# Performance work log

Measured on AMD Instinct MI355X. Metric: run time of the kernel, lower is better.

Reference implementation:

```python
import jax, jax.numpy as jnp
import numpy as np

N_LEAVES = 16384
D = 1024
L = 32


def _build_full_binary_tree(n_leaves):
    # Leaves are node ids [0, n_leaves); internal nodes are assigned ids level by
    # level bottom-up, so children always have smaller ids than their parent and
    # left_idx/right_idx are grouped contiguously per level.
    level_nodes = np.arange(n_leaves)
    nid = n_leaves
    lefts, rights = [], []
    while level_nodes.size > 1:
        lefts.append(level_nodes[0::2])
        rights.append(level_nodes[1::2])
        w = level_nodes.size // 2
        level_nodes = np.arange(nid, nid + w)
        nid += w
    return np.concatenate(lefts).astype(np.int32), np.concatenate(rights).astype(np.int32)


def setup_inputs() -> dict:
    key = jax.random.key(0)
    k_h, k_t, k_w = jax.random.split(key, 3)
    n_nodes = 2 * N_LEAVES - 1
    hidden = jax.random.normal(k_h, (n_nodes, D), dtype=jnp.float32)
    # xavier_normal-ish scales
    trans = jax.random.normal(k_t, (L, L), dtype=jnp.float32) * (2.0 / (L + L)) ** 0.5
    W_pred = jax.random.normal(k_w, (L, 2 * D), dtype=jnp.float32) * (2.0 / (2 * D + L)) ** 0.5
    b_pred = jnp.zeros((L,), dtype=jnp.float32)
    left_idx, right_idx = _build_full_binary_tree(N_LEAVES)
    return {
        "hidden": hidden,
        "trans": trans,
        "W_pred": W_pred,
        "b_pred": b_pred,
        "left_idx": jnp.asarray(left_idx),
        "right_idx": jnp.asarray(right_idx),
    }


def reference(hidden, trans, W_pred, b_pred, left_idx, right_idx):
    # hidden: [N, D] node bottom-up hidden states; N = 2*n_leaves - 1
    n_nodes, d = hidden.shape
    n_leaves = (n_nodes + 1) // 2
    num_labels = trans.shape[0]

    # collect_avg_hidden: mean over all node hidden states
    avg_h = jnp.mean(hidden, axis=0)  # [D]
    # avg_h_pred: emission = Linear(concat(h, avg_h))  -> [N, L]
    feats = jnp.concatenate(
        [hidden, jnp.broadcast_to(avg_h, hidden.shape)], axis=1
    )  # [N, 2D]
    emission = feats @ W_pred.T + b_pred  # [N, L]

    # Inside DP, bottom-up, batched by tree level. For an internal node p:
    #   inside[p, y] = logsumexp_{l,r}( emission[p,y] + trans[y,l] + inside_left[l]
    #                                   + trans[y,r] + inside_right[r] )
    # which factorizes exactly into two independent logsumexps.
    scores = jnp.zeros((n_nodes, num_labels), dtype=hidden.dtype)
    scores = scores.at[:n_leaves].set(emission[:n_leaves])

    pos = 0
    node_base = n_leaves
    width = n_leaves // 2
    while width >= 1:  # fixed log2(n_leaves) structural levels
        li = left_idx[pos:pos + width]
        ri = right_idx[pos:pos + width]
        ls = scores[li]  # [width, L]
        rs = scores[ri]  # [width, L]
        # trans[y, c] + child_score[c], logsumexp over child label c
        left_m = jax.nn.logsumexp(trans[None, :, :] + ls[:, None, :], axis=2)
        right_m = jax.nn.logsumexp(trans[None, :, :] + rs[:, None, :], axis=2)
        new = emission[node_base:node_base + width] + left_m + right_m
        scores = scores.at[node_base:node_base + width].set(new)
        pos += width
        node_base += width
        width //= 2

    return scores[n_nodes - 1]  # root inside score, [L]
```

## Files before the change

kernel.cpp:

```cpp
#include <hip/hip_runtime.h>

#define NN 32767
#define NL 16384
#define DD 1024
#define LL 32

typedef __attribute__((ext_vector_type(8))) short bf16x8;
typedef __attribute__((ext_vector_type(4))) float f32x4;

__device__ __forceinline__ short f2bf(float f) {
  union { float f; unsigned u; } x; x.f = f;
  unsigned r = x.u + 0x7FFFu + ((x.u >> 16) & 1u);
  return (short)(r >> 16);
}

__device__ __forceinline__ bf16x8 cvt8(float4 a, float4 b) {
  bf16x8 r;
  r[0] = f2bf(a.x); r[1] = f2bf(a.y); r[2] = f2bf(a.z); r[3] = f2bf(a.w);
  r[4] = f2bf(b.x); r[5] = f2bf(b.y); r[6] = f2bf(b.z); r[7] = f2bf(b.w);
  return r;
}

__device__ __forceinline__ void gld_lds16(const float* g, float* l) {
  __builtin_amdgcn_global_load_lds(
      (const __attribute__((address_space(1))) void*)g,
      (__attribute__((address_space(3))) void*)l, 16, 0, 0);
}

__global__ __launch_bounds__(256) void pack_kernel(const float* __restrict__ Wp,
                                                   short* __restrict__ Wpk) {
  int idx = blockIdx.x * 256 + threadIdx.x;
  #pragma unroll
  for (int t = 0; t < 4; ++t, idx += 16384) {
    const int j = idx & 7, m = (idx >> 3) & 3, lane = (idx >> 5) & 63, s = idx >> 11;
    const int wrow = (lane & 15) + 16 * (m & 1);
    const int wcol = (m >> 1) * 1024 + s * 32 + (lane >> 4) * 8 + j;
    Wpk[idx] = f2bf(Wp[(size_t)wrow * (2 * DD) + wcol]);
  }
}

__global__ __launch_bounds__(256) void gemm_kernel(
    const float* __restrict__ hidden, const short* __restrict__ Wpk,
    float* __restrict__ E0, float* __restrict__ gpart) {
  __shared__ float lds[4 * 3 * 1024];
  const int tid = threadIdx.x;
  const int wid = tid >> 6, lane = tid & 63;
  const int tile = blockIdx.x * 4 + wid;
  const int mrow = lane & 15, g = lane >> 4;
  const int swz = (mrow & 7) << 4;
  float* ldsw = lds + wid * 3072;

  const float* ab0; const float* ab1; const float* ab2; const float* ab3;
  {
    const int lr = lane >> 4, lc16 = (lane & 15) * 16;
    #define MKAB(I, P) { const int row = (I)*4 + lr;                         \
      const int csrc = lc16 ^ ((row & 7) << 4);                              \
      int grow = tile * 16 + row; if (grow > NN - 1) grow = NN - 1;          \
      P = hidden + (size_t)grow * DD + (csrc >> 2); }
    MKAB(0, ab0) MKAB(1, ab1) MKAB(2, ab2) MKAB(3, ab3)
    #undef MKAB
  }
  const bf16x8* wbase = (const bf16x8*)Wpk + (size_t)lane * 4;

  const int cidx00 = ((g * 32) ^ swz) >> 2;
  const int cidx01 = ((g * 32 + 16) ^ swz) >> 2;
  const int cidx10 = ((128 + g * 32) ^ swz) >> 2;
  const int cidx11 = ((128 + g * 32 + 16) ^ swz) >> 2;

  f32x4 acc0 = {0,0,0,0}, acc1 = {0,0,0,0}, acc2 = {0,0,0,0}, acc3 = {0,0,0,0};

#define STAGE_A(KC) {                                   \
    float* ld_ = ldsw + ((KC) % 3) * 1024;              \
    gld_lds16(ab0 + (KC) * 64, ld_);                    \
    gld_lds16(ab1 + (KC) * 64, ld_ + 256);              \
    gld_lds16(ab2 + (KC) * 64, ld_ + 512);              \
    gld_lds16(ab3 + (KC) * 64, ld_ + 768); }

#define LOAD_W(KC, W0,W1,W2,W3, X0,X1,X2,X3) {          \
    const bf16x8* p_ = wbase + (size_t)(2 * (KC)) * 256; \
    W0 = p_[0];   W1 = p_[1];   W2 = p_[2];   W3 = p_[3]; \
    X0 = p_[256]; X1 = p_[257]; X2 = p_[258]; X3 = p_[259]; }

#define CHUNK(KC, VM, W0,W1,W2,W3, X0,X1,X2,X3)                              \
  { if ((KC) + 2 < 16) STAGE_A((KC) + 2)                                     \
    asm volatile("s_waitcnt vmcnt(" VM ")" ::: "memory");                    \
    { const float* bc = ldsw + ((KC) % 3) * 1024 + mrow * 64;                \
      float4 fa0 = *(const float4*)(bc + cidx00);                            \
      float4 fb0 = *(const float4*)(bc + cidx01);                            \
      bf16x8 af0 = cvt8(fa0, fb0);                                           \
      acc0 = __builtin_amdgcn_mfma_f32_16x16x32_bf16(af0, W0, acc0, 0,0,0);  \
      acc1 = __builtin_amdgcn_mfma_f32_16x16x32_bf16(af0, W1, acc1, 0,0,0);  \
      acc2 = __builtin_amdgcn_mfma_f32_16x16x32_bf16(af0, W2, acc2, 0,0,0);  \
      acc3 = __builtin_amdgcn_mfma_f32_16x16x32_bf16(af0, W3, acc3, 0,0,0);  \
      float4 fa1 = *(const float4*)(bc + cidx10);                            \
      float4 fb1 = *(const float4*)(bc + cidx11);                            \
      bf16x8 af1 = cvt8(fa1, fb1);                                           \
      acc0 = __builtin_amdgcn_mfma_f32_16x16x32_bf16(af1, X0, acc0, 0,0,0);  \
      acc1 = __builtin_amdgcn_mfma_f32_16x16x32_bf16(af1, X1, acc1, 0,0,0);  \
      acc2 = __builtin_amdgcn_mfma_f32_16x16x32_bf16(af1, X2, acc2, 0,0,0);  \
      acc3 = __builtin_amdgcn_mfma_f32_16x16x32_bf16(af1, X3, acc3, 0,0,0);  \
    }                                                                        \
    if ((KC) + 2 < 16) LOAD_W((KC) + 2, W0,W1,W2,W3, X0,X1,X2,X3) }

  bf16x8 u0,u1,u2,u3,u4,u5,u6,u7, v0,v1,v2,v3,v4,v5,v6,v7;
  STAGE_A(0) STAGE_A(1)
  LOAD_W(0, u0,u1,u2,u3, u4,u5,u6,u7)
  LOAD_W(1, v0,v1,v2,v3, v4,v5,v6,v7)
  CHUNK( 0, "24", u0,u1,u2,u3, u4,u5,u6,u7)
  CHUNK( 1, "32", v0,v1,v2,v3, v4,v5,v6,v7)
  CHUNK( 2, "24", u0,u1,u2,u3, u4,u5,u6,u7)
  CHUNK( 3, "24", v0,v1,v2,v3, v4,v5,v6,v7)
  CHUNK( 4, "24", u0,u1,u2,u3, u4,u5,u6,u7)
  CHUNK( 5, "24", v0,v1,v2,v3, v4,v5,v6,v7)
  CHUNK( 6, "24", u0,u1,u2,u3, u4,u5,u6,u7)
  CHUNK( 7, "24", v0,v1,v2,v3, v4,v5,v6,v7)
  CHUNK( 8, "24", u0,u1,u2,u3, u4,u5,u6,u7)
  CHUNK( 9, "24", v0,v1,v2,v3, v4,v5,v6,v7)
  CHUNK(10, "24", u0,u1,u2,u3, u4,u5,u6,u7)
  CHUNK(11, "24", v0,v1,v2,v3, v4,v5,v6,v7)
  CHUNK(12, "24", u0,u1,u2,u3, u4,u5,u6,u7)
  CHUNK(13, "24", v0,v1,v2,v3, v4,v5,v6,v7)
  CHUNK(14, "20", u0,u1,u2,u3, u4,u5,u6,u7)
  CHUNK(15, "8",  v0,v1,v2,v3, v4,v5,v6,v7)
#undef CHUNK
#undef LOAD_W
#undef STAGE_A

  #pragma unroll
  for (int r = 0; r < 4; ++r) {
    const int srow = tile * 16 + g * 4 + r;
    if (srow < NN) {
      E0[(size_t)srow * LL + mrow]      = acc0[r];
      E0[(size_t)srow * LL + mrow + 16] = acc1[r];
    }
  }
  if (tile == 2047 && g == 3) { acc2[3] = 0.f; acc3[3] = 0.f; }
  float s2 = acc2[0] + acc2[1] + acc2[2] + acc2[3];
  float s3 = acc3[0] + acc3[1] + acc3[2] + acc3[3];
  s2 += __shfl_xor(s2, 16, 64); s2 += __shfl_xor(s2, 32, 64);
  s3 += __shfl_xor(s3, 16, 64); s3 += __shfl_xor(s3, 32, 64);
  if (lane < 32) gpart[(size_t)tile * LL + lane] = (lane < 16) ? s2 : s3;
}

__global__ __launch_bounds__(256) void cvec_kernel(
    const float* __restrict__ bp, const float* __restrict__ gpart,
    float* __restrict__ cvec) {
  const int col = blockIdx.x;
  const int tid = threadIdx.x, wid = tid >> 6, lane = tid & 63;
  float s = 0.f;
  for (int w = tid; w < 2048; w += 256) s += gpart[(size_t)w * LL + col];
  #pragma unroll
  for (int m = 1; m <= 32; m <<= 1) s += __shfl_xor(s, m, 64);
  __shared__ float red[4];
  if (lane == 0) red[wid] = s;
  __syncthreads();
  if (tid == 0)
    cvec[col] = bp[col] + (red[0] + red[1] + red[2] + red[3]) * (1.0f / (float)NN);
}

__device__ __forceinline__ float lse32(const float4* tt, const float4* sv) {
  float m = -3.0e38f;
  float4 v[8];
  #pragma unroll
  for (int i = 0; i < 8; ++i) {
    float4 t = tt[i], s = sv[i], w;
    w.x = t.x + s.x; w.y = t.y + s.y; w.z = t.z + s.z; w.w = t.w + s.w;
    v[i] = w;
    m = fmaxf(m, fmaxf(fmaxf(w.x, w.y), fmaxf(w.z, w.w)));
  }
  float ss = 0.f;
  #pragma unroll
  for (int i = 0; i < 8; ++i) {
    ss += __expf(v[i].x - m) + __expf(v[i].y - m) +
          __expf(v[i].z - m) + __expf(v[i].w - m);
  }
  return m + __logf(ss);
}

__global__ __launch_bounds__(1024) void tree_kernel(
    const float* __restrict__ E0, const float* __restrict__ cvec,
    const float* __restrict__ trans, const float* __restrict__ src,
    float* __restrict__ dst, int base1, int leafmode) {
  __shared__ float l1[16][LL], l2[8][LL], l3[4][LL];
  const int wid = threadIdx.x >> 6, lane = threadIdx.x & 63;
  const int j = lane & 31, half = lane >> 5;
  const int b = blockIdx.x, G = gridDim.x;
  float4 tt[8];
  #pragma unroll
  for (int i = 0; i < 8; ++i) tt[i] = *(const float4*)(trans + j * LL + i * 4);
  const float cj = cvec[j];
  float4 sv[8];

  {
    const int n = b * 16 + wid;
    const float* sp = src + (size_t)(2 * n + half) * LL;
    if (leafmode) {
      #pragma unroll
      for (int i = 0; i < 8; ++i) {
        float4 vv = *(const float4*)(sp + i * 4);
        float4 c4 = *(const float4*)(cvec + i * 4);
        vv.x += c4.x; vv.y += c4.y; vv.z += c4.z; vv.w += c4.w;
        sv[i] = vv;
      }
    } else {
      #pragma unroll
      for (int i = 0; i < 8; ++i) sv[i] = *(const float4*)(sp + i * 4);
    }
    float lsum = lse32(tt, sv);
    float other = __shfl_xor(lsum, 32, 64);
    float o = E0[(size_t)(base1 + n) * LL + j] + cj + lsum + other;
    if (lane < 32) l1[wid][j] = o;
  }
  __syncthreads();
  const int base2 = base1 + G * 16;
  if (wid < 8) {
    const float* sp = l1[2 * wid + half];
    #pragma unroll
    for (int i = 0; i < 8; ++i) sv[i] = *(const float4*)(sp + i * 4);
    float lsum = lse32(tt, sv);
    float other = __shfl_xor(lsum, 32, 64);
    float o = E0[(size_t)(base2 + b * 8 + wid) * LL + j] + cj + lsum + other;
    if (lane < 32) l2[wid][j] = o;
  }
  __syncthreads();
  const int base3 = base2 + G * 8;
  if (wid < 4) {
    const float* sp = l2[2 * wid + half];
    #pragma unroll
    for (int i = 0; i < 8; ++i) sv[i] = *(const float4*)(sp + i * 4);
    float lsum = lse32(tt, sv);
    float other = __shfl_xor(lsum, 32, 64);
    float o = E0[(size_t)(base3 + b * 4 + wid) * LL + j] + cj + lsum + other;
    if (lane < 32) l3[wid][j] = o;
  }
  __syncthreads();
  const int base4 = base3 + G * 4;
  if (wid < 2) {
    const float* sp = l3[2 * wid + half];
    #pragma unroll
    for (int i = 0; i < 8; ++i) sv[i] = *(const float4*)(sp + i * 4);
    float lsum = lse32(tt, sv);
    float other = __shfl_xor(lsum, 32, 64);
    float o = E0[(size_t)(base4 + b * 2 + wid) * LL + j] + cj + lsum + other;
    if (lane < 32) l1[wid][j] = o;
  }
  __syncthreads();
  const int base5 = base4 + G * 2;
  if (wid == 0) {
    const float* sp = l1[half];
    #pragma unroll
    for (int i = 0; i < 8; ++i) sv[i] = *(const float4*)(sp + i * 4);
    float lsum = lse32(tt, sv);
    float other = __shfl_xor(lsum, 32, 64);
    float o = E0[(size_t)(base5 + b) * LL + j] + cj + lsum + other;
    if (lane < 32) dst[(size_t)b * LL + j] = o;
  }
}

__global__ __launch_bounds__(512) void tail_kernel(
    const float* __restrict__ E0, const float* __restrict__ cvec,
    const float* __restrict__ trans, const float* __restrict__ S10,
    float* __restrict__ out) {
  __shared__ float t1[8][LL], t2[4][LL], t3[2][LL];
  const int wid = threadIdx.x >> 6, lane = threadIdx.x & 63;
  const int j = lane & 31, half = lane >> 5;
  float4 tt[8];
  #pragma unroll
  for (int i = 0; i < 8; ++i) tt[i] = *(const float4*)(trans + j * LL + i * 4);
  const float cj = cvec[j];
  float4 sv[8];

  {
    const float* sp = S10 + (size_t)(2 * wid + half) * LL;
    #pragma unroll
    for (int i = 0; i < 8; ++i) sv[i] = *(const float4*)(sp + i * 4);
    float lsum = lse32(tt, sv);
    float other = __shfl_xor(lsum, 32, 64);
    float o = E0[(size_t)(32752 + wid) * LL + j] + cj + lsum + other;
    if (lane < 32) t1[wid][j] = o;
  }
  __syncthreads();
  if (wid < 4) {
    const float* sp = t1[2 * wid + half];
    #pragma unroll
    for (int i = 0; i < 8; ++i) sv[i] = *(const float4*)(sp + i * 4);
    float lsum = lse32(tt, sv);
    float other = __shfl_xor(lsum, 32, 64);
    float o = E0[(size_t)(32760 + wid) * LL + j] + cj + lsum + other;
    if (lane < 32) t2[wid][j] = o;
  }
  __syncthreads();
  if (wid < 2) {
    const float* sp = t2[2 * wid + half];
    #pragma unroll
    for (int i = 0; i < 8; ++i) sv[i] = *(const float4*)(sp + i * 4);
    float lsum = lse32(tt, sv);
    float other = __shfl_xor(lsum, 32, 64);
    float o = E0[(size_t)(32764 + wid) * LL + j] + cj + lsum + other;
    if (lane < 32) t3[wid][j] = o;
  }
  __syncthreads();
  if (wid == 0) {
    const float* sp = t3[half];
    #pragma unroll
    for (int i = 0; i < 8; ++i) sv[i] = *(const float4*)(sp + i * 4);
    float lsum = lse32(tt, sv);
    float other = __shfl_xor(lsum, 32, 64);
    float o = E0[(size_t)32766 * LL + j] + cj + lsum + other;
    if (lane < 32) out[j] = o;
  }
}

extern "C" void kernel_launch(void* const* d_in, const int* in_sizes, int n_in,
                              void* d_out, int out_size, void* d_ws, size_t ws_size,
                              hipStream_t stream) {
  const float* hidden = (const float*)d_in[0];
  const float* trans  = (const float*)d_in[1];
  const float* Wp     = (const float*)d_in[2];
  const float* bp     = (const float*)d_in[3];

  float* ws    = (float*)d_ws;
  float* E0    = ws;
  float* gpart = E0 + (size_t)NN * LL;
  float* cvecb = gpart + (size_t)2048 * LL;
  float* S5    = cvecb + 32;
  float* S10   = S5 + 512 * LL;
  short* Wpk   = (short*)(S10 + 16 * LL);

  pack_kernel<<<64, 256, 0, stream>>>(Wp, Wpk);
  gemm_kernel<<<512, 256, 0, stream>>>(hidden, Wpk, E0, gpart);
  cvec_kernel<<<32, 256, 0, stream>>>(bp, gpart, cvecb);
  tree_kernel<<<512, 1024, 0, stream>>>(E0, cvecb, trans, E0, S5, 16384, 1);
  tree_kernel<<<16, 1024, 0, stream>>>(E0, cvecb, trans, S5, S10, 32256, 0);
  tail_kernel<<<1, 512, 0, stream>>>(E0, cvecb, trans, S10, (float*)d_out);
}
```

Before: 73.26 us.

## Reformulate tree logsumexp as exp-trans dot product and merge upper-level kernels

Replaces the per-lane 32-term logsumexp with a factorised form: each lane takes a wave max over child scores, exponentiates its own score once, shares the values through LDS, and dots them with a precomputed exp(trans) row before a single log. This cuts the exp count per node from 32 to one. The second tree kernel and the tail kernel are merged into a single one-block kernel that processes the top nine levels, removing a launch. The risk is numerical: exp(trans) times exp(score minus max) can underflow when entries differ widely, and the single block now serialises more levels.

```diff
diff --git a/kernel.cpp b/kernel.cpp
--- a/kernel.cpp
+++ b/kernel.cpp
@@ -1,4 +1,5 @@
 #include <hip/hip_runtime.h>
+
 
 #define NN 32767
 #define NL 16384
@@ -158,155 +159,195 @@
     cvec[col] = bp[col] + (red[0] + red[1] + red[2] + red[3]) * (1.0f / (float)NN);
 }
 
-__device__ __forceinline__ float lse32(const float4* tt, const float4* sv) {
-  float m = -3.0e38f;
-  float4 v[8];
-  #pragma unroll
-  for (int i = 0; i < 8; ++i) {
-    float4 t = tt[i], s = sv[i], w;
-    w.x = t.x + s.x; w.y = t.y + s.y; w.z = t.z + s.z; w.w = t.w + s.w;
-    v[i] = w;
-    m = fmaxf(m, fmaxf(fmaxf(w.x, w.y), fmaxf(w.z, w.w)));
-  }
-  float ss = 0.f;
-  #pragma unroll
-  for (int i = 0; i < 8; ++i) {
-    ss += __expf(v[i].x - m) + __expf(v[i].y - m) +
-          __expf(v[i].z - m) + __expf(v[i].w - m);
-  }
-  return m + __logf(ss);
-}
-
-__global__ __launch_bounds__(1024) void tree_kernel(
+
+__device__ __forceinline__ float node_combine(float cs, float ep, float cvj,
+                                              const float4* etr, float* eswb,
+                                              int lane) {
+  float m = cs;
+  #pragma unroll
+  for (int d = 1; d <= 16; d <<= 1) m = fmaxf(m, __shfl_xor(m, d, 64));
+  float es = __expf(cs - m);
+  eswb[lane] = es;
+  asm volatile("s_waitcnt lgkmcnt(0)" ::: "memory");
+  __builtin_amdgcn_sched_barrier(0);
+  const float4* eb = (const float4*)(eswb + (lane & 32));
+  float a0 = 0.f, a1 = 0.f, a2 = 0.f, a3 = 0.f;
+  #pragma unroll
+  for (int i = 0; i < 8; i += 2) {
+    float4 e0 = eb[i], e1 = eb[i + 1];
+    float4 t0 = etr[i], t1 = etr[i + 1];
+    a0 += t0.x * e0.x; a1 += t0.y * e0.y; a2 += t0.z * e0.z; a3 += t0.w * e0.w;
+    a0 += t1.x * e1.x; a1 += t1.y * e1.y; a2 += t1.z * e1.z; a3 += t1.w * e1.w;
+  }
+  float dot = (a0 + a1) + (a2 + a3);
+  float lseh = m + __logf(dot);
+  float oth = __shfl_xor(lseh, 32, 64);
+  return ep + cvj + lseh + oth;
+}
+
+#define LOAD_ETR(etr, trans, lane)                                        \
+  _Pragma("unroll")                                                       \
+  for (int i_ = 0; i_ < 8; ++i_) {                                        \
+    float4 t_ = *(const float4*)((trans) + ((lane) & 31) * LL + i_ * 4);  \
+    etr[i_].x = __expf(t_.x); etr[i_].y = __expf(t_.y);                   \
+    etr[i_].z = __expf(t_.z); etr[i_].w = __expf(t_.w);                   \
+  }
+
+__global__ __launch_bounds__(1024) void tree1_kernel(
     const float* __restrict__ E0, const float* __restrict__ cvec,
-    const float* __restrict__ trans, const float* __restrict__ src,
-    float* __restrict__ dst, int base1, int leafmode) {
-  __shared__ float l1[16][LL], l2[8][LL], l3[4][LL];
-  const int wid = threadIdx.x >> 6, lane = threadIdx.x & 63;
+    const float* __restrict__ trans, float* __restrict__ S5) {
+  __shared__ float esb[16][64];
+  __shared__ float l1[16][LL], l2[8][LL], l3[4][LL], l4[2][LL];
+  const int tid = threadIdx.x, w = tid >> 6, lane = tid & 63;
+  const int j = lane & 31, half = lane >> 5, b = blockIdx.x;
+  float4 etr[8];
+  LOAD_ETR(etr, trans, lane)
+  const float cvj = cvec[j];
+  float* eswb = esb[w];
+
+  {
+    const int n = b * 16 + w;
+    float cs = E0[(size_t)(2 * n + half) * LL + j] + cvj;
+    float ep = E0[(size_t)(16384 + n) * LL + j];
+    float o = node_combine(cs, ep, cvj, etr, eswb, lane);
+    if (lane < 32) l1[w][j] = o;
+  }
+  __syncthreads();
+  if (w < 8) {
+    float cs = l1[2 * w + half][j];
+    float ep = E0[(size_t)(24576 + b * 8 + w) * LL + j];
+    float o = node_combine(cs, ep, cvj, etr, eswb, lane);
+    if (lane < 32) l2[w][j] = o;
+  }
+  __syncthreads();
+  if (w < 4) {
+    float cs = l2[2 * w + half][j];
+    float ep = E0[(size_t)(28672 + b * 4 + w) * LL + j];
+    float o = node_combine(cs, ep, cvj, etr, eswb, lane);
+    if (lane < 32) l3[w][j] = o;
+  }
+  __syncthreads();
+  if (w < 2) {
+    float cs = l3[2 * w + half][j];
+    float ep = E0[(size_t)(30720 + b * 2 + w) * LL + j];
+    float o = node_combine(cs, ep, cvj, etr, eswb, lane);
+    if (lane < 32) l4[w][j] = o;
+  }
+  __syncthreads();
+  if (w == 0) {
+    float cs = l4[half][j];
+    float ep = E0[(size_t)(31744 + b) * LL + j];
+    float o = node_combine(cs, ep, cvj, etr, eswb, lane);
+    if (lane < 32) S5[(size_t)b * LL + j] = o;
+  }
+}
+
+__global__ __launch_bounds__(1024) void tree2_kernel(
+    const float* __restrict__ E0, const float* __restrict__ cvec,
+    const float* __restrict__ trans, const float* __restrict__ S5,
+    float* __restrict__ out) {
+  __shared__ float esb[16][64];
+  __shared__ float bufA[256][LL];
+  __shared__ float bufB[128][LL];
+  const int tid = threadIdx.x, w = tid >> 6, lane = tid & 63;
   const int j = lane & 31, half = lane >> 5;
-  const int b = blockIdx.x, G = gridDim.x;
-  float4 tt[8];
-  #pragma unroll
-  for (int i = 0; i < 8; ++i) tt[i] = *(const float4*)(trans + j * LL + i * 4);
-  const float cj = cvec[j];
-  float4 sv[8];
-
-  {
-    const int n = b * 16 + wid;
-    const float* sp = src + (size_t)(2 * n + half) * LL;
-    if (leafmode) {
-      #pragma unroll
-      for (int i = 0; i < 8; ++i) {
-        float4 vv = *(const float4*)(sp + i * 4);
-        float4 c4 = *(const float4*)(cvec + i * 4);
-        vv.x += c4.x; vv.y += c4.y; vv.z += c4.z; vv.w += c4.w;
-        sv[i] = vv;
-      }
-    } else {
-      #pragma unroll
-      for (int i = 0; i < 8; ++i) sv[i] = *(const float4*)(sp + i * 4);
-    }
-    float lsum = lse32(tt, sv);
-    float other = __shfl_xor(lsum, 32, 64);
-    float o = E0[(size_t)(base1 + n) * LL + j] + cj + lsum + other;
-    if (lane < 32) l1[wid][j] = o;
-  }
-  __syncthreads();
-  const int base2 = base1 + G * 16;
-  if (wid < 8) {
-    const float* sp = l1[2 * wid + half];
-    #pragma unroll
-    for (int i = 0; i < 8; ++i) sv[i] = *(const float4*)(sp + i * 4);
-    float lsum = lse32(tt, sv);
-    float other = __shfl_xor(lsum, 32, 64);
-    float o = E0[(size_t)(base2 + b * 8 + wid) * LL + j] + cj + lsum + other;
-    if (lane < 32) l2[wid][j] = o;
-  }
-  __syncthreads();
-  const int base3 = base2 + G * 8;
-  if (wid < 4) {
-    const float* sp = l2[2 * wid + half];
-    #pragma unroll
-    for (int i = 0; i < 8; ++i) sv[i] = *(const float4*)(sp + i * 4);
-    float lsum = lse32(tt, sv);
-    float other = __shfl_xor(lsum, 32, 64);
-    float o = E0[(size_t)(base3 + b * 4 + wid) * LL + j] + cj + lsum + other;
-    if (lane < 32) l3[wid][j] = o;
-  }
-  __syncthreads();
-  const int base4 = base3 + G * 4;
-  if (wid < 2) {
-    const float* sp = l3[2 * wid + half];
-    #pragma unroll
-    for (int i = 0; i < 8; ++i) sv[i] = *(const float4*)(sp + i * 4);
-    float lsum = lse32(tt, sv);
-    float other = __shfl_xor(lsum, 32, 64);
-    float o = E0[(size_t)(base4 + b * 2 + wid) * LL + j] + cj + lsum + other;
-    if (lane < 32) l1[wid][j] = o;
-  }
-  __syncthreads();
-  const int base5 = base4 + G * 2;
-  if (wid == 0) {
-    const float* sp = l1[half];
-    #pragma unroll
-    for (int i = 0; i < 8; ++i) sv[i] = *(const float4*)(sp + i * 4);
-    float lsum = lse32(tt, sv);
-    float other = __shfl_xor(lsum, 32, 64);
-    float o = E0[(size_t)(base5 + b) * LL + j] + cj + lsum + other;
-    if (lane < 32) dst[(size_t)b * LL + j] = o;
-  }
-}
-
-__global__ __launch_bounds__(512) void tail_kernel(
-    const float* __restrict__ E0, const float* __restrict__ cvec,
-    const float* __restrict__ trans, const float* __restrict__ S10,
-    float* __restrict__ out) {
-  __shared__ float t1[8][LL], t2[4][LL], t3[2][LL];
-  const int wid = threadIdx.x >> 6, lane = threadIdx.x & 63;
-  const int j = lane & 31, half = lane >> 5;
-  float4 tt[8];
-  #pragma unroll
-  for (int i = 0; i < 8; ++i) tt[i] = *(const float4*)(trans + j * LL + i * 4);
-  const float cj = cvec[j];
-  float4 sv[8];
-
-  {
-    const float* sp = S10 + (size_t)(2 * wid + half) * LL;
-    #pragma unroll
-    for (int i = 0; i < 8; ++i) sv[i] = *(const float4*)(sp + i * 4);
-    float lsum = lse32(tt, sv);
-    float other = __shfl_xor(lsum, 32, 64);
-    float o = E0[(size_t)(32752 + wid) * LL + j] + cj + lsum + other;
-    if (lane < 32) t1[wid][j] = o;
-  }
-  __syncthreads();
-  if (wid < 4) {
-    const float* sp = t1[2 * wid + half];
-    #pragma unroll
-    for (int i = 0; i < 8; ++i) sv[i] = *(const float4*)(sp + i * 4);
-    float lsum = lse32(tt, sv);
-    float other = __shfl_xor(lsum, 32, 64);
-    float o = E0[(size_t)(32760 + wid) * LL + j] + cj + lsum + other;
-    if (lane < 32) t2[wid][j] = o;
-  }
-  __syncthreads();
-  if (wid < 2) {
-    const float* sp = t2[2 * wid + half];
-    #pragma unroll
-    for (int i = 0; i < 8; ++i) sv[i] = *(const float4*)(sp + i * 4);
-    float lsum = lse32(tt, sv);
-    float other = __shfl_xor(lsum, 32, 64);
-    float o = E0[(size_t)(32764 + wid) * LL + j] + cj + lsum + other;
-    if (lane < 32) t3[wid][j] = o;
-  }
-  __syncthreads();
-  if (wid == 0) {
-    const float* sp = t3[half];
-    #pragma unroll
-    for (int i = 0; i < 8; ++i) sv[i] = *(const float4*)(sp + i * 4);
-    float lsum = lse32(tt, sv);
-    float other = __shfl_xor(lsum, 32, 64);
-    float o = E0[(size_t)32766 * LL + j] + cj + lsum + other;
+  float4 etr[8];
+  LOAD_ETR(etr, trans, lane)
+  const float cvj = cvec[j];
+  float* eswb = esb[w];
+
+  {
+    float cs[16], ep[16];
+    #pragma unroll
+    for (int t = 0; t < 16; ++t) {
+      const int n = w * 16 + t;
+      cs[t] = S5[(size_t)(2 * n + half) * LL + j];
+      ep[t] = E0[(size_t)(32256 + n) * LL + j];
+    }
+    #pragma unroll
+    for (int t = 0; t < 16; ++t) {
+      float o = node_combine(cs[t], ep[t], cvj, etr, eswb, lane);
+      if (lane < 32) bufA[w * 16 + t][j] = o;
+    }
+  }
+  __syncthreads();
+  {
+    float cs[8], ep[8];
+    #pragma unroll
+    for (int t = 0; t < 8; ++t) {
+      const int n = w * 8 + t;
+      cs[t] = bufA[2 * n + half][j];
+      ep[t] = E0[(size_t)(32512 + n) * LL + j];
+    }
+    #pragma unroll
+    for (int t = 0; t < 8; ++t) {
+      float o = node_combine(cs[t], ep[t], cvj, etr, eswb, lane);
+      if (lane < 32) bufB[w * 8 + t][j] = o;
+    }
+  }
+  __syncthreads();
+  {
+    float cs[4], ep[4];
+    #pragma unroll
+    for (int t = 0; t < 4; ++t) {
+      const int n = w * 4 + t;
+      cs[t] = bufB[2 * n + half][j];
+      ep[t] = E0[(size_t)(32640 + n) * LL + j];
+    }
+    #pragma unroll
+    for (int t = 0; t < 4; ++t) {
+      float o = node_combine(cs[t], ep[t], cvj, etr, eswb, lane);
+      if (lane < 32) bufA[w * 4 + t][j] = o;
+    }
+  }
+  __syncthreads();
+  {
+    float cs[2], ep[2];
+    #pragma unroll
+    for (int t = 0; t < 2; ++t) {
+      const int n = w * 2 + t;
+      cs[t] = bufA[2 * n + half][j];
+      ep[t] = E0[(size_t)(32704 + n) * LL + j];
+    }
+    #pragma unroll
+    for (int t = 0; t < 2; ++t) {
+      float o = node_combine(cs[t], ep[t], cvj, etr, eswb, lane);
+      if (lane < 32) bufB[w * 2 + t][j] = o;
+    }
+  }
+  __syncthreads();
+  {
+    float cs = bufB[2 * w + half][j];
+    float ep = E0[(size_t)(32736 + w) * LL + j];
+    float o = node_combine(cs, ep, cvj, etr, eswb, lane);
+    if (lane < 32) bufA[w][j] = o;
+  }
+  __syncthreads();
+  if (w < 8) {
+    float cs = bufA[2 * w + half][j];
+    float ep = E0[(size_t)(32752 + w) * LL + j];
+    float o = node_combine(cs, ep, cvj, etr, eswb, lane);
+    if (lane < 32) bufB[w][j] = o;
+  }
+  __syncthreads();
+  if (w < 4) {
+    float cs = bufB[2 * w + half][j];
+    float ep = E0[(size_t)(32760 + w) * LL + j];
+    float o = node_combine(cs, ep, cvj, etr, eswb, lane);
+    if (lane < 32) bufA[w][j] = o;
+  }
+  __syncthreads();
+  if (w < 2) {
+    float cs = bufA[2 * w + half][j];
+    float ep = E0[(size_t)(32764 + w) * LL + j];
+    float o = node_combine(cs, ep, cvj, etr, eswb, lane);
+    if (lane < 32) bufB[w][j] = o;
+  }
+  __syncthreads();
+  if (w == 0) {
+    float cs = bufB[half][j];
+    float ep = E0[(size_t)32766 * LL + j];
+    float o = node_combine(cs, ep, cvj, etr, eswb, lane);
     if (lane < 32) out[j] = o;
   }
 }
@@ -324,13 +365,11 @@
   float* gpart = E0 + (size_t)NN * LL;
   float* cvecb = gpart + (size_t)2048 * LL;
   float* S5    = cvecb + 32;
-  float* S10   = S5 + 512 * LL;
-  short* Wpk   = (short*)(S10 + 16 * LL);
+  short* Wpk   = (short*)(S5 + 512 * LL);
 
   pack_kernel<<<64, 256, 0, stream>>>(Wp, Wpk);
   gemm_kernel<<<512, 256, 0, stream>>>(hidden, Wpk, E0, gpart);
   cvec_kernel<<<32, 256, 0, stream>>>(bp, gpart, cvecb);
-  tree_kernel<<<512, 1024, 0, stream>>>(E0, cvecb, trans, E0, S5, 16384, 1);
-  tree_kernel<<<16, 1024, 0, stream>>>(E0, cvecb, trans, S5, S10, 32256, 0);
-  tail_kernel<<<1, 512, 0, stream>>>(E0, cvecb, trans, S10, (float*)d_out);
-}
+  tree1_kernel<<<512, 1024, 0, stream>>>(E0, cvecb, trans, S5);
+  tree2_kernel<<<1, 1024, 0, stream>>>(E0, cvecb, trans, S5, (float*)d_out);
+}
```

Measured after the change: 81.25 us. 1.11x slower.

## Fuse upper tree levels and tail into one single-block kernel

Applied to the files above, without the earlier changes.

Replaces the second tree_kernel launch (16 blocks) and the tail kernel with one 1024-thread block that runs the last nine tree levels from S5 to the root, keeping intermediate levels in shared memory. Each node's logsumexp is rewritten as max plus log of a dot product between exp(trans), precomputed once per lane, and exp-shifted child scores staged through LDS. This removes one kernel launch and the S10 round trip through global memory. The cost is that the wide level (512 to 256 nodes) now runs serially on one CU instead of across 16 blocks.

```diff
diff --git a/kernel.cpp b/kernel.cpp
--- a/kernel.cpp
+++ b/kernel.cpp
@@ -1,4 +1,5 @@
 #include <hip/hip_runtime.h>
+
 
 #define NN 32767
 #define NL 16384
@@ -257,56 +258,139 @@
   }
 }
 
-__global__ __launch_bounds__(512) void tail_kernel(
+__device__ __forceinline__ float node_es(float cs, float ep, float cvj,
+                                         const float4* etr, float* esrow,
+                                         int lane) {
+  float m = cs;
+  #pragma unroll
+  for (int d = 1; d <= 16; d <<= 1) m = fmaxf(m, __shfl_xor(m, d, 64));
+  float es = __expf(cs - m);
+  esrow[lane] = es;
+  const float4* eb = (const float4*)(esrow + (lane & 32));
+  float a0 = 0.f, a1 = 0.f, a2 = 0.f, a3 = 0.f;
+  #pragma unroll
+  for (int i = 0; i < 8; ++i) {
+    float4 e = eb[i], t = etr[i];
+    a0 += t.x * e.x; a1 += t.y * e.y; a2 += t.z * e.z; a3 += t.w * e.w;
+  }
+  float lseh = m + __logf((a0 + a1) + (a2 + a3));
+  float oth = __shfl_xor(lseh, 32, 64);
+  return ep + cvj + lseh + oth;
+}
+
+#define LOAD_ETR(etr, trans, lane)                                        \
+  _Pragma("unroll")                                                       \
+  for (int i_ = 0; i_ < 8; ++i_) {                                        \
+    float4 t_ = *(const float4*)((trans) + ((lane) & 31) * LL + i_ * 4);  \
+    etr[i_].x = __expf(t_.x); etr[i_].y = __expf(t_.y);                   \
+    etr[i_].z = __expf(t_.z); etr[i_].w = __expf(t_.w);                   \
+  }
+
+__global__ __launch_bounds__(1024) void tree2_kernel(
     const float* __restrict__ E0, const float* __restrict__ cvec,
-    const float* __restrict__ trans, const float* __restrict__ S10,
+    const float* __restrict__ trans, const float* __restrict__ S5,
     float* __restrict__ out) {
-  __shared__ float t1[8][LL], t2[4][LL], t3[2][LL];
-  const int wid = threadIdx.x >> 6, lane = threadIdx.x & 63;
+  __shared__ float esb[16][2][64];
+  __shared__ float bufA[256][LL];
+  __shared__ float bufB[128][LL];
+  const int tid = threadIdx.x, w = tid >> 6, lane = tid & 63;
   const int j = lane & 31, half = lane >> 5;
-  float4 tt[8];
-  #pragma unroll
-  for (int i = 0; i < 8; ++i) tt[i] = *(const float4*)(trans + j * LL + i * 4);
-  const float cj = cvec[j];
-  float4 sv[8];
-
-  {
-    const float* sp = S10 + (size_t)(2 * wid + half) * LL;
-    #pragma unroll
-    for (int i = 0; i < 8; ++i) sv[i] = *(const float4*)(sp + i * 4);
-    float lsum = lse32(tt, sv);
-    float other = __shfl_xor(lsum, 32, 64);
-    float o = E0[(size_t)(32752 + wid) * LL + j] + cj + lsum + other;
-    if (lane < 32) t1[wid][j] = o;
-  }
-  __syncthreads();
-  if (wid < 4) {
-    const float* sp = t1[2 * wid + half];
-    #pragma unroll
-    for (int i = 0; i < 8; ++i) sv[i] = *(const float4*)(sp + i * 4);
-    float lsum = lse32(tt, sv);
-    float other = __shfl_xor(lsum, 32, 64);
-    float o = E0[(size_t)(32760 + wid) * LL + j] + cj + lsum + other;
-    if (lane < 32) t2[wid][j] = o;
-  }
-  __syncthreads();
-  if (wid < 2) {
-    const float* sp = t2[2 * wid + half];
-    #pragma unroll
-    for (int i = 0; i < 8; ++i) sv[i] = *(const float4*)(sp + i * 4);
-    float lsum = lse32(tt, sv);
-    float other = __shfl_xor(lsum, 32, 64);
-    float o = E0[(size_t)(32764 + wid) * LL + j] + cj + lsum + other;
-    if (lane < 32) t3[wid][j] = o;
-  }
-  __syncthreads();
-  if (wid == 0) {
-    const float* sp = t3[half];
-    #pragma unroll
-    for (int i = 0; i < 8; ++i) sv[i] = *(const float4*)(sp + i * 4);
-    float lsum = lse32(tt, sv);
-    float other = __shfl_xor(lsum, 32, 64);
-    float o = E0[(size_t)32766 * LL + j] + cj + lsum + other;
+  float4 etr[8];
+  LOAD_ETR(etr, trans, lane)
+  const float cvj = cvec[j];
+
+  {
+    float cs[16], ep[16];
+    #pragma unroll
+    for (int t = 0; t < 16; ++t) {
+      const int n = w * 16 + t;
+      cs[t] = S5[(size_t)(2 * n + half) * LL + j];
+      ep[t] = E0[(size_t)(32256 + n) * LL + j];
+    }
+    #pragma unroll
+    for (int t = 0; t < 16; ++t) {
+      float o = node_es(cs[t], ep[t], cvj, etr, esb[w][t & 1], lane);
+      if (lane < 32) bufA[w * 16 + t][j] = o;
+    }
+  }
+  __syncthreads();
+  {
+    float cs[8], ep[8];
+    #pragma unroll
+    for (int t = 0; t < 8; ++t) {
+      const int n = w * 8 + t;
+      cs[t] = bufA[2 * n + half][j];
+      ep[t] = E0[(size_t)(32512 + n) * LL + j];
+    }
+    #pragma unroll
+    for (int t = 0; t < 8; ++t) {
+      float o = node_es(cs[t], ep[t], cvj, etr, esb[w][t & 1], lane);
+      if (lane < 32) bufB[w * 8 + t][j] = o;
+    }
+  }
+  __syncthreads();
+  {
+    float cs[4], ep[4];
+    #pragma unroll
+    for (int t = 0; t < 4; ++t) {
+      const int n = w * 4 + t;
+      cs[t] = bufB[2 * n + half][j];
+      ep[t] = E0[(size_t)(32640 + n) * LL + j];
+    }
+    #pragma unroll
+    for (int t = 0; t < 4; ++t) {
+      float o = node_es(cs[t], ep[t], cvj, etr, esb[w][t & 1], lane);
+      if (lane < 32) bufA[w * 4 + t][j] = o;
+    }
+  }
+  __syncthreads();
+  {
+    float cs[2], ep[2];
+    #pragma unroll
+    for (int t = 0; t < 2; ++t) {
+      const int n = w * 2 + t;
+      cs[t] = bufA[2 * n + half][j];
+      ep[t] = E0[(size_t)(32704 + n) * LL + j];
+    }
+    #pragma unroll
+    for (int t = 0; t < 2; ++t) {
+      float o = node_es(cs[t], ep[t], cvj, etr, esb[w][t & 1], lane);
+      if (lane < 32) bufB[w * 2 + t][j] = o;
+    }
+  }
+  __syncthreads();
+  {
+    float cs = bufB[2 * w + half][j];
+    float ep = E0[(size_t)(32736 + w) * LL + j];
+    float o = node_es(cs, ep, cvj, etr, esb[w][0], lane);
+    if (lane < 32) bufA[w][j] = o;
+  }
+  __syncthreads();
+  if (w < 8) {
+    float cs = bufA[2 * w + half][j];
+    float ep = E0[(size_t)(32752 + w) * LL + j];
+    float o = node_es(cs, ep, cvj, etr, esb[w][0], lane);
+    if (lane < 32) bufB[w][j] = o;
+  }
+  __syncthreads();
+  if (w < 4) {
+    float cs = bufB[2 * w + half][j];
+    float ep = E0[(size_t)(32760 + w) * LL + j];
+    float o = node_es(cs, ep, cvj, etr, esb[w][0], lane);
+    if (lane < 32) bufA[w][j] = o;
+  }
+  __syncthreads();
+  if (w < 2) {
+    float cs = bufA[2 * w + half][j];
+    float ep = E0[(size_t)(32764 + w) * LL + j];
+    float o = node_es(cs, ep, cvj, etr, esb[w][0], lane);
+    if (lane < 32) bufB[w][j] = o;
+  }
+  __syncthreads();
+  if (w == 0) {
+    float cs = bufB[half][j];
+    float ep = E0[(size_t)32766 * LL + j];
+    float o = node_es(cs, ep, cvj, etr, esb[0][0], lane);
     if (lane < 32) out[j] = o;
   }
 }
@@ -324,13 +408,11 @@
   float* gpart = E0 + (size_t)NN * LL;
   float* cvecb = gpart + (size_t)2048 * LL;
   float* S5    = cvecb + 32;
-  float* S10   = S5 + 512 * LL;
-  short* Wpk   = (short*)(S10 + 16 * LL);
+  short* Wpk   = (short*)(S5 + 512 * LL);
 
   pack_kernel<<<64, 256, 0, stream>>>(Wp, Wpk);
   gemm_kernel<<<512, 256, 0, stream>>>(hidden, Wpk, E0, gpart);
   cvec_kernel<<<32, 256, 0, stream>>>(bp, gpart, cvecb);
   tree_kernel<<<512, 1024, 0, stream>>>(E0, cvecb, trans, E0, S5, 16384, 1);
-  tree_kernel<<<16, 1024, 0, stream>>>(E0, cvecb, trans, S5, S10, 32256, 0);
-  tail_kernel<<<1, 512, 0, stream>>>(E0, cvecb, trans, S10, (float*)d_out);
-}
+  tree2_kernel<<<1, 1024, 0, stream>>>(E0, cvecb, trans, S5, (float*)d_out);
+}
```

Measured after the change: 85.72 us. +17.0%, slower.
